# Optimization experiments

Hardware: AMD Instinct MI355X
Metric: run time of the kernel (lower is better)

## Reference

```python
import jax, jax.numpy as jnp
import numpy as np

D_MODEL = 1024


def bitlinear(x, weight):
    # ternary quantization with straight-through estimator; forward value is w_q*scale
    scale = jnp.clip(jnp.mean(jnp.abs(weight), axis=1, keepdims=True), 1e-5, None)
    w_q = jnp.clip(jnp.round(weight / scale), -1.0, 1.0)
    w = weight + jax.lax.stop_gradient(w_q * scale - weight)
    return x @ w.T


def rmsnorm(x, w, eps=1e-6):
    return x * jax.lax.rsqrt(jnp.mean(x * x, axis=-1, keepdims=True) + eps) * w


def setup_inputs() -> dict:
    key = jax.random.key(0)
    ks = jax.random.split(key, 6)
    D = D_MODEL
    std = np.sqrt(2.0 / D)  # kaiming_normal fan_out
    return {
        "x": jax.random.normal(ks[0], (4, 4096, D), dtype=jnp.float32),
        "Wr": jax.random.normal(ks[1], (D, D), dtype=jnp.float32) * std,
        "Wk": jax.random.normal(ks[2], (D, D), dtype=jnp.float32) * std,
        "Wv": jax.random.normal(ks[3], (D, D), dtype=jnp.float32) * std,
        "Wo": jax.random.normal(ks[4], (D, D), dtype=jnp.float32) * std,
        "decay": jnp.ones((D,), dtype=jnp.float32) * 0.99,
        "ln_w": jnp.ones((D,), dtype=jnp.float32),
    }


def reference(x, Wr, Wk, Wv, Wo, decay, ln_w):
    B, T, D = x.shape
    r = jax.nn.sigmoid(bitlinear(x, Wr))
    k = bitlinear(x, Wk)
    v = bitlinear(x, Wv)
    dec = jax.nn.sigmoid(decay)                              # [D]
    kv = k * v                                               # [B,T,D]
    positions = jnp.arange(T, dtype=x.dtype)                 # [T]
    log_decay = jnp.log(jnp.clip(dec, 1e-7, None))           # [D]
    scale = jnp.exp(positions[:, None] * log_decay[None, :])  # [T,D]
    scaled = kv / jnp.clip(scale, 1e-10, None)[None]         # [B,T,D]
    cum = jnp.cumsum(scaled, axis=1)                         # [B,T,D]
    state = cum * scale[None]                                # [B,T,D]
    return bitlinear(rmsnorm(r * state, ln_w), Wo)
```

## Files before the change

### kernel.cpp

```cpp
#include <hip/hip_runtime.h>

typedef unsigned short u16;
typedef __attribute__((ext_vector_type(8))) short bf16x8;
typedef __attribute__((ext_vector_type(4))) float f32x4;
typedef __attribute__((ext_vector_type(4))) int   i32x4;
typedef __attribute__((ext_vector_type(4))) unsigned short u16x4;

#define DM 1024

__device__ __forceinline__ float bf2f(u16 u){
  union { unsigned int i; float f; } v; v.i = ((unsigned int)u)<<16; return v.f;
}
__device__ __forceinline__ u16 f2bf(float f){
  unsigned int x = __float_as_uint(f);
  return (u16)((x + 0x7FFFu + ((x>>16)&1u)) >> 16);
}

__global__ __launch_bounds__(256)
void quantize_w(const float* __restrict__ W0, const float* __restrict__ W1,
                const float* __restrict__ W2, const float* __restrict__ W3,
                u16* __restrict__ wq, signed char* __restrict__ wq8,
                float* __restrict__ wsc)
{
  const int gr   = blockIdx.x*4 + (threadIdx.x>>6);
  const int lane = threadIdx.x & 63;
  const float* W; int row;
  if (gr < 1024)      { W = W0; row = gr; }
  else if (gr < 3072) { row = (gr-1024)>>1; W = (gr&1) ? W2 : W1; }
  else                { W = W3; row = gr-3072; }
  const float* wr = W + (size_t)row*DM;
  float4 v[4]; float s = 0.f;
  #pragma unroll
  for (int c=0;c<4;c++){
    v[c] = *(const float4*)&wr[c*256 + lane*4];
    s += fabsf(v[c].x)+fabsf(v[c].y)+fabsf(v[c].z)+fabsf(v[c].w);
  }
  #pragma unroll
  for (int off=32; off; off>>=1) s += __shfl_down(s, off);
  s = __shfl(s, 0);
  const float scale = fmaxf(s*(1.f/1024.f), 1e-5f);
  if (lane==0) wsc[gr] = scale;
  if (gr < 3072){
    u16* wo = wq + (size_t)gr*DM;
    #pragma unroll
    for (int c=0;c<4;c++){
      u16x4 q;
      q[0] = f2bf(fminf(fmaxf(rintf(v[c].x/scale),-1.f),1.f));
      q[1] = f2bf(fminf(fmaxf(rintf(v[c].y/scale),-1.f),1.f));
      q[2] = f2bf(fminf(fmaxf(rintf(v[c].z/scale),-1.f),1.f));
      q[3] = f2bf(fminf(fmaxf(rintf(v[c].w/scale),-1.f),1.f));
      *(u16x4*)&wo[c*256 + lane*4] = q;
    }
  } else {
    signed char* wo = wq8 + (size_t)(gr-3072)*DM;
    #pragma unroll
    for (int c=0;c<4;c++){
      const int q0 = (int)rintf(fminf(fmaxf(v[c].x/scale,-1.f),1.f));
      const int q1 = (int)rintf(fminf(fmaxf(v[c].y/scale,-1.f),1.f));
      const int q2 = (int)rintf(fminf(fmaxf(v[c].z/scale,-1.f),1.f));
      const int q3 = (int)rintf(fminf(fmaxf(v[c].w/scale,-1.f),1.f));
      const unsigned int p = (q0&0xFF) | ((q1&0xFF)<<8) | ((q2&0xFF)<<16) | ((unsigned)(q3&0xFF)<<24);
      *(unsigned int*)&wo[c*256 + lane*4] = p;
    }
  }
}

__global__ void cvt_x(const float* __restrict__ x, u16* __restrict__ xb){
  const int i = (blockIdx.x*256 + threadIdx.x)*4;
  float4 v = *(const float4*)&x[i];
  u16x4 o; o[0]=f2bf(v.x); o[1]=f2bf(v.y); o[2]=f2bf(v.z); o[3]=f2bf(v.w);
  *(u16x4*)&xb[i] = o;
}

#define RD(base, off) (*(const bf16x8*)((const char*)(base) + (off)))

__global__ __launch_bounds__(256, 4)
void gemm_rkv(const u16* __restrict__ Ag, const u16* __restrict__ Bq,
              const float* __restrict__ bscale,
              u16* __restrict__ o_r, u16* __restrict__ o_kv)
{
  __shared__ u16 sA[128*64];
  __shared__ u16 sB[128*64];
  const int tid = threadIdx.x, wave = tid>>6, lane = tid&63;
  const int lr = lane&15, lg = lane>>4;
  const int wm = wave>>1, wn = wave&1;
  const int bm0 = blockIdx.x*128, bn0 = blockIdx.y*128;
  constexpr int nt = 16;

  const int r8   = lane>>3;
  const int scol = ((lane&7)<<4) ^ (r8<<4);
  const size_t aoff = (size_t)(bm0 + wave*8 + r8)*2048 + scol;
  const size_t boff = (size_t)(bn0 + wave*8 + r8)*2048 + scol;
  const int ldst = wave*1024;

  const int S = (lr&7)<<4;
  const int koff0 = ((lg<<4)     ) ^ S;
  const int koff1 = (64 + (lg<<4)) ^ S;
  const int arow = (wm*64 + lr)*128;
  const int brow = (wn*64 + lr)*128;

  f32x4 acc[4][4];
  #pragma unroll
  for (int i=0;i<4;i++)
    #pragma unroll
    for (int j=0;j<4;j++) acc[i][j] = (f32x4){0.f,0.f,0.f,0.f};

  for (int t=0; t<nt; ++t){
    #pragma unroll
    for (int q=0;q<4;q++){
      __builtin_amdgcn_global_load_lds(
        (const __attribute__((address_space(1))) void*)((const char*)Ag + aoff + q*65536 + (size_t)t*128),
        (__attribute__((address_space(3))) void*)((char*)sA + ldst + q*4096), 16, 0, 0);
      __builtin_amdgcn_global_load_lds(
        (const __attribute__((address_space(1))) void*)((const char*)Bq + boff + q*65536 + (size_t)t*128),
        (__attribute__((address_space(3))) void*)((char*)sB + ldst + q*4096), 16, 0, 0);
    }
    __syncthreads();
    {
      bf16x8 a[4], b[4];
      #pragma unroll
      for (int m=0;m<4;m++) a[m] = RD(sA, arow + m*2048 + koff0);
      #pragma unroll
      for (int n=0;n<4;n++) b[n] = RD(sB, brow + n*2048 + koff0);
      #pragma unroll
      for (int m=0;m<4;m++)
        #pragma unroll
        for (int n=0;n<4;n++)
          acc[m][n] = __builtin_amdgcn_mfma_f32_16x16x32_bf16(a[m], b[n], acc[m][n], 0,0,0);
      #pragma unroll
      for (int m=0;m<4;m++) a[m] = RD(sA, arow + m*2048 + koff1);
      #pragma unroll
      for (int n=0;n<4;n++) b[n] = RD(sB, brow + n*2048 + koff1);
      #pragma unroll
      for (int m=0;m<4;m++)
        #pragma unroll
        for (int n=0;n<4;n++)
          acc[m][n] = __builtin_amdgcn_mfma_f32_16x16x32_bf16(a[m], b[n], acc[m][n], 0,0,0);
    }
    __syncthreads();
  }

  #pragma unroll
  for (int mi=0; mi<4; ++mi){
    #pragma unroll
    for (int ni=0; ni<4; ++ni){
      const int col = bn0 + wn*64 + ni*16 + lr;
      const float sc = bscale[col];
      const int rowb = bm0 + wm*64 + mi*16 + lg*4;
      const f32x4 a = acc[mi][ni];
      if (bn0 < 1024){
        #pragma unroll
        for (int r2=0;r2<4;r2++){
          const float val = a[r2]*sc;
          o_r[(size_t)(rowb+r2)*DM + col] = f2bf(1.f/(1.f+expf(-val)));
        }
      } else {
        const int dv = (col - 1024) >> 1;
        #pragma unroll
        for (int r2=0;r2<4;r2++){
          const float val = a[r2]*sc;
          const float pr  = val * __shfl_xor(val, 1);
          if (!(lr & 1))
            o_kv[(size_t)(rowb+r2)*DM + dv] = f2bf(pr);
        }
      }
    }
  }
}

#define RD8(base, off) (*(const i32x4*)((const char*)(base) + (off)))

__global__ __launch_bounds__(256, 4)
void gemm_o8(const signed char* __restrict__ Ag, const signed char* __restrict__ Bq,
             const float* __restrict__ bscale, const float* __restrict__ sxr,
             float* __restrict__ o_f)
{
  __shared__ signed char sA[128*128];
  __shared__ signed char sB[128*128];
  const int tid = threadIdx.x, wave = tid>>6, lane = tid&63;
  const int lr = lane&15, lg = lane>>4;
  const int wm = wave>>1, wn = wave&1;
  const int bm0 = blockIdx.x*128, bn0 = blockIdx.y*128;
  constexpr int nt = 8;

  const int r8   = lane>>3;
  const int scol = ((lane&7)<<4) ^ (r8<<4);
  const size_t aoff = (size_t)(bm0 + wave*8 + r8)*1024 + scol;
  const size_t boff = (size_t)(bn0 + wave*8 + r8)*1024 + scol;
  const int ldst = wave*1024;

  const int S = (lr&7)<<4;
  const int koff0 = ((lg<<4)     ) ^ S;
  const int koff1 = (64 + (lg<<4)) ^ S;
  const int arow = (wm*64 + lr)*128;
  const int brow = (wn*64 + lr)*128;

  i32x4 acc[4][4];
  #pragma unroll
  for (int i=0;i<4;i++)
    #pragma unroll
    for (int j=0;j<4;j++) acc[i][j] = (i32x4){0,0,0,0};

  for (int t=0; t<nt; ++t){
    #pragma unroll
    for (int q=0;q<4;q++){
      __builtin_amdgcn_global_load_lds(
        (const __attribute__((address_space(1))) void*)((const char*)Ag + aoff + q*32768 + (size_t)t*128),
        (__attribute__((address_space(3))) void*)((char*)sA + ldst + q*4096), 16, 0, 0);
      __builtin_amdgcn_global_load_lds(
        (const __attribute__((address_space(1))) void*)((const char*)Bq + boff + q*32768 + (size_t)t*128),
        (__attribute__((address_space(3))) void*)((char*)sB + ldst + q*4096), 16, 0, 0);
    }
    __syncthreads();
    {
      i32x4 a[4], b[4];
      #pragma unroll
      for (int m=0;m<4;m++) a[m] = RD8(sA, arow + m*2048 + koff0);
      #pragma unroll
      for (int n=0;n<4;n++) b[n] = RD8(sB, brow + n*2048 + koff0);
      #pragma unroll
      for (int m=0;m<4;m++)
        #pragma unroll
        for (int n=0;n<4;n++)
          acc[m][n] = __builtin_amdgcn_mfma_i32_16x16x64_i8(a[m], b[n], acc[m][n], 0,0,0);
      #pragma unroll
      for (int m=0;m<4;m++) a[m] = RD8(sA, arow + m*2048 + koff1);
      #pragma unroll
      for (int n=0;n<4;n++) b[n] = RD8(sB, brow + n*2048 + koff1);
      #pragma unroll
      for (int m=0;m<4;m++)
        #pragma unroll
        for (int n=0;n<4;n++)
          acc[m][n] = __builtin_amdgcn_mfma_i32_16x16x64_i8(a[m], b[n], acc[m][n], 0,0,0);
    }
    __syncthreads();
  }

  #pragma unroll
  for (int mi=0; mi<4; ++mi){
    const int rowb = bm0 + wm*64 + mi*16 + lg*4;
    float sx[4];
    #pragma unroll
    for (int r2=0;r2<4;r2++) sx[r2] = sxr[rowb+r2];
    #pragma unroll
    for (int ni=0; ni<4; ++ni){
      const int col = bn0 + wn*64 + ni*16 + lr;
      const float sc = bscale[col];
      const i32x4 a = acc[mi][ni];
      #pragma unroll
      for (int r2=0;r2<4;r2++)
        o_f[(size_t)(rowb+r2)*DM + col] = (float)a[r2] * sx[r2] * sc;
    }
  }
}

__global__ __launch_bounds__(256)
void kv_phase1(const u16* __restrict__ kv, const float* __restrict__ decay,
               float* __restrict__ part)
{
  const int c = blockIdx.x & 127, b = blockIdx.x >> 7;
  const int d0 = threadIdx.x*4;
  float ld[4]; f32x4 sum = {0.f,0.f,0.f,0.f};
  #pragma unroll
  for (int j=0;j<4;j++){
    const float dec = 1.f/(1.f+expf(-decay[d0+j]));
    ld[j] = logf(fmaxf(dec, 1e-7f));
  }
  for (int t=c*32; t<c*32+32; ++t){
    const size_t base = ((size_t)(b*4096 + t))*DM + d0;
    const u16x4 p4 = *(const u16x4*)&kv[base];
    const float tf = (float)t;
    #pragma unroll
    for (int j=0;j<4;j++){
      const float e = expf(tf*ld[j]);
      sum[j] += bf2f(p4[j]) / fmaxf(e, 1e-10f);
    }
  }
  *(f32x4*)&part[((size_t)(b*128+c))*DM + d0] = sum;
}

__global__ void chunk_prefix(float* __restrict__ part){
  const int g = blockIdx.x*256 + threadIdx.x;
  const int b = g >> 10, d = g & 1023;
  float run = 0.f;
  for (int c8=0; c8<128; c8+=8){
    float v[8];
    #pragma unroll
    for (int i=0;i<8;i++)
      v[i] = part[((size_t)(b*128+c8+i))*DM + d];
    #pragma unroll
    for (int i=0;i<8;i++){
      const float tmp = v[i];
      part[((size_t)(b*128+c8+i))*DM + d] = run;
      run += tmp;
    }
  }
}

__global__ __launch_bounds__(256)
void scan_norm(const u16* __restrict__ kv, const u16* __restrict__ rbuf,
               const float* __restrict__ part, const float* __restrict__ decay,
               const float* __restrict__ lnw, signed char* __restrict__ yn8,
               float* __restrict__ sxr)
{
  const int c = blockIdx.x & 127, b = blockIdx.x >> 7;
  const int tid = threadIdx.x, lane = tid&63, wave = tid>>6;
  const int d0 = tid*4;
  __shared__ float redS[2][4];
  __shared__ float redM[2][4];
  f32x4 run = *(const f32x4*)&part[((size_t)(b*128+c))*DM + d0];
  float ld[4], lw[4];
  #pragma unroll
  for (int j=0;j<4;j++){
    const float dec = 1.f/(1.f+expf(-decay[d0+j]));
    ld[j] = logf(fmaxf(dec, 1e-7f));
    lw[j] = lnw[d0+j];
  }
  for (int t=c*32; t<c*32+32; ++t){
    const size_t base = ((size_t)(b*4096+t))*DM + d0;
    const u16x4 p4 = *(const u16x4*)&kv[base];
    const u16x4 r4 = *(const u16x4*)&rbuf[base];
    const float tf = (float)t;
    float yl[4]; float ss = 0.f, mx = 0.f;
    #pragma unroll
    for (int j=0;j<4;j++){
      const float e = expf(tf*ld[j]);
      run[j] += bf2f(p4[j]) / fmaxf(e, 1e-10f);
      const float st = run[j]*e;
      const float y = bf2f(r4[j])*st;
      ss += y*y;
      yl[j] = y*lw[j];
      mx = fmaxf(mx, fabsf(yl[j]));
    }
    #pragma unroll
    for (int off=32; off; off>>=1){
      ss += __shfl_down(ss, off);
      mx  = fmaxf(mx, __shfl_down(mx, off));
    }
    if (lane==0){ redS[t&1][wave] = ss; redM[t&1][wave] = mx; }
    __builtin_amdgcn_s_barrier();
    const float tot = (redS[t&1][0]+redS[t&1][1])+(redS[t&1][2]+redS[t&1][3]);
    const float m1  = fmaxf(fmaxf(redM[t&1][0],redM[t&1][1]),
                            fmaxf(redM[t&1][2],redM[t&1][3]));
    const float rs  = 1.f/sqrtf(tot*(1.f/1024.f) + 1e-6f);
    const float m1s = fmaxf(m1, 1e-30f);
    const float qk  = 127.f/m1s;
    if (tid==0) sxr[b*4096+t] = m1s*rs*(1.f/127.f);
    unsigned int p = 0;
    #pragma unroll
    for (int j=0;j<4;j++){
      int q = (int)rintf(yl[j]*qk);
      q = q>127?127:(q<-127?-127:q);
      p |= ((unsigned)(q&0xFF)) << (8*j);
    }
    *(unsigned int*)&yn8[base] = p;
  }
}

extern "C" void kernel_launch(void* const* d_in, const int* in_sizes, int n_in,
                              void* d_out, int out_size, void* d_ws, size_t ws_size,
                              hipStream_t stream)
{
  (void)in_sizes; (void)n_in; (void)out_size; (void)ws_size;
  const float* x    = (const float*)d_in[0];
  const float* Wr   = (const float*)d_in[1];
  const float* Wk   = (const float*)d_in[2];
  const float* Wv   = (const float*)d_in[3];
  const float* Wo   = (const float*)d_in[4];
  const float* dec  = (const float*)d_in[5];
  const float* lnw  = (const float*)d_in[6];

  char* ws = (char*)d_ws;
  u16*         wq    = (u16*)(ws + 0);
  signed char* wq8   = (signed char*)(ws + 6291456);
  float*       wsc   = (float*)(ws + 7340032);
  u16*         rbuf  = (u16*)(ws + 7356416);
  u16*         kvbuf = (u16*)(ws + 40910848);
  float*       part  = (float*)(ws + 74465280);
  u16*         xb    = (u16*)(ws + 76562432);
  signed char* yn8   = (signed char*)(ws + 110116864);
  float*       sxr   = (float*)(ws + 126894080);

  quantize_w<<<1024, 256, 0, stream>>>(Wr, Wk, Wv, Wo, wq, wq8, wsc);
  cvt_x<<<16384, 256, 0, stream>>>(x, xb);
  gemm_rkv<<<dim3(128,24), 256, 0, stream>>>(xb, wq, wsc, rbuf, kvbuf);
  kv_phase1<<<512, 256, 0, stream>>>(kvbuf, dec, part);
  chunk_prefix<<<16, 256, 0, stream>>>(part);
  scan_norm<<<512, 256, 0, stream>>>(kvbuf, rbuf, part, dec, lnw, yn8, sxr);
  gemm_o8<<<dim3(128,8), 256, 0, stream>>>(yn8, wq8, wsc + 3072, sxr, (float*)d_out);
}
```

Before: 221.6 us.

## Fuse chunk partial sums into GEMM epilogue and merge weight/x packing launches

Computes the per-32-timestep decayed kv chunk sums directly in the gemm_rkv epilogue using shuffle reductions, which removes the kv_phase1 kernel and its re-read of the kv buffer. It also merges weight quantization and x bf16 conversion into one launch. The epilogue now runs extra expf and divide work per element and adds register pressure in a kernel bounded at 4 waves per SIMD. Summation order changes slightly because it uses bf16-unrounded products rather than the stored bf16 values.

```diff
diff --git a/kernel.cpp b/kernel.cpp
--- a/kernel.cpp
+++ b/kernel.cpp
@@ -17,11 +17,19 @@
 }
 
 __global__ __launch_bounds__(256)
-void quantize_w(const float* __restrict__ W0, const float* __restrict__ W1,
-                const float* __restrict__ W2, const float* __restrict__ W3,
-                u16* __restrict__ wq, signed char* __restrict__ wq8,
-                float* __restrict__ wsc)
-{
+void init_pack(const float* __restrict__ W0, const float* __restrict__ W1,
+               const float* __restrict__ W2, const float* __restrict__ W3,
+               const float* __restrict__ x,
+               u16* __restrict__ wq, signed char* __restrict__ wq8,
+               float* __restrict__ wsc, u16* __restrict__ xb)
+{
+  if (blockIdx.x >= 1024){
+    const int i = ((blockIdx.x-1024)*256 + threadIdx.x)*4;
+    float4 v = *(const float4*)&x[i];
+    u16x4 o; o[0]=f2bf(v.x); o[1]=f2bf(v.y); o[2]=f2bf(v.z); o[3]=f2bf(v.w);
+    *(u16x4*)&xb[i] = o;
+    return;
+  }
   const int gr   = blockIdx.x*4 + (threadIdx.x>>6);
   const int lane = threadIdx.x & 63;
   const float* W; int row;
@@ -65,19 +73,13 @@
   }
 }
 
-__global__ void cvt_x(const float* __restrict__ x, u16* __restrict__ xb){
-  const int i = (blockIdx.x*256 + threadIdx.x)*4;
-  float4 v = *(const float4*)&x[i];
-  u16x4 o; o[0]=f2bf(v.x); o[1]=f2bf(v.y); o[2]=f2bf(v.z); o[3]=f2bf(v.w);
-  *(u16x4*)&xb[i] = o;
-}
-
 #define RD(base, off) (*(const bf16x8*)((const char*)(base) + (off)))
 
 __global__ __launch_bounds__(256, 4)
 void gemm_rkv(const u16* __restrict__ Ag, const u16* __restrict__ Bq,
-              const float* __restrict__ bscale,
-              u16* __restrict__ o_r, u16* __restrict__ o_kv)
+              const float* __restrict__ bscale, const float* __restrict__ decay,
+              u16* __restrict__ o_r, u16* __restrict__ o_kv,
+              float* __restrict__ part)
 {
   __shared__ u16 sA[128*64];
   __shared__ u16 sB[128*64];
@@ -141,28 +143,48 @@
   }
 
   #pragma unroll
-  for (int mi=0; mi<4; ++mi){
-    #pragma unroll
-    for (int ni=0; ni<4; ++ni){
-      const int col = bn0 + wn*64 + ni*16 + lr;
-      const float sc = bscale[col];
-      const int rowb = bm0 + wm*64 + mi*16 + lg*4;
-      const f32x4 a = acc[mi][ni];
-      if (bn0 < 1024){
+  for (int ni=0; ni<4; ++ni){
+    const int col = bn0 + wn*64 + ni*16 + lr;
+    const float sc = bscale[col];
+    if (bn0 < 1024){
+      #pragma unroll
+      for (int mi=0; mi<4; ++mi){
+        const int rowb = bm0 + wm*64 + mi*16 + lg*4;
+        const f32x4 a = acc[mi][ni];
         #pragma unroll
         for (int r2=0;r2<4;r2++){
           const float val = a[r2]*sc;
           o_r[(size_t)(rowb+r2)*DM + col] = f2bf(1.f/(1.f+expf(-val)));
         }
-      } else {
-        const int dv = (col - 1024) >> 1;
+      }
+    } else {
+      const int dv  = (col - 1024) >> 1;
+      const float dec = 1.f/(1.f+expf(-decay[dv]));
+      const float ldv = logf(fmaxf(dec, 1e-7f));
+      float s0 = 0.f, s1 = 0.f;
+      #pragma unroll
+      for (int mi=0; mi<4; ++mi){
+        const int rowb = bm0 + wm*64 + mi*16 + lg*4;
+        const f32x4 a = acc[mi][ni];
         #pragma unroll
         for (int r2=0;r2<4;r2++){
           const float val = a[r2]*sc;
           const float pr  = val * __shfl_xor(val, 1);
           if (!(lr & 1))
             o_kv[(size_t)(rowb+r2)*DM + dv] = f2bf(pr);
+          const int tt = (rowb & 4095) + r2;
+          const float e = expf((float)tt * ldv);
+          const float sv = pr / fmaxf(e, 1e-10f);
+          if (mi < 2) s0 += sv; else s1 += sv;
         }
+      }
+      s0 += __shfl_down(s0, 32); s0 += __shfl_down(s0, 16);
+      s1 += __shfl_down(s1, 32); s1 += __shfl_down(s1, 16);
+      if ((lane < 16) && !(lane & 1)){
+        const int bb = bm0 >> 12;
+        const int c0 = ((bm0 & 4095) + wm*64) >> 5;
+        part[((size_t)(bb*128 + c0    ))*DM + dv] = s0;
+        part[((size_t)(bb*128 + c0 + 1))*DM + dv] = s1;
       }
     }
   }
@@ -252,31 +274,6 @@
         o_f[(size_t)(rowb+r2)*DM + col] = (float)a[r2] * sx[r2] * sc;
     }
   }
-}
-
-__global__ __launch_bounds__(256)
-void kv_phase1(const u16* __restrict__ kv, const float* __restrict__ decay,
-               float* __restrict__ part)
-{
-  const int c = blockIdx.x & 127, b = blockIdx.x >> 7;
-  const int d0 = threadIdx.x*4;
-  float ld[4]; f32x4 sum = {0.f,0.f,0.f,0.f};
-  #pragma unroll
-  for (int j=0;j<4;j++){
-    const float dec = 1.f/(1.f+expf(-decay[d0+j]));
-    ld[j] = logf(fmaxf(dec, 1e-7f));
-  }
-  for (int t=c*32; t<c*32+32; ++t){
-    const size_t base = ((size_t)(b*4096 + t))*DM + d0;
-    const u16x4 p4 = *(const u16x4*)&kv[base];
-    const float tf = (float)t;
-    #pragma unroll
-    for (int j=0;j<4;j++){
-      const float e = expf(tf*ld[j]);
-      sum[j] += bf2f(p4[j]) / fmaxf(e, 1e-10f);
-    }
-  }
-  *(f32x4*)&part[((size_t)(b*128+c))*DM + d0] = sum;
 }
 
 __global__ void chunk_prefix(float* __restrict__ part){
@@ -381,10 +378,8 @@
   signed char* yn8   = (signed char*)(ws + 110116864);
   float*       sxr   = (float*)(ws + 126894080);
 
-  quantize_w<<<1024, 256, 0, stream>>>(Wr, Wk, Wv, Wo, wq, wq8, wsc);
-  cvt_x<<<16384, 256, 0, stream>>>(x, xb);
-  gemm_rkv<<<dim3(128,24), 256, 0, stream>>>(xb, wq, wsc, rbuf, kvbuf);
-  kv_phase1<<<512, 256, 0, stream>>>(kvbuf, dec, part);
+  init_pack<<<17408, 256, 0, stream>>>(Wr, Wk, Wv, Wo, x, wq, wq8, wsc, xb);
+  gemm_rkv<<<dim3(128,24), 256, 0, stream>>>(xb, wq, wsc, dec, rbuf, kvbuf, part);
   chunk_prefix<<<16, 256, 0, stream>>>(part);
   scan_norm<<<512, 256, 0, stream>>>(kvbuf, rbuf, part, dec, lnw, yn8, sxr);
   gemm_o8<<<dim3(128,8), 256, 0, stream>>>(yn8, wq8, wsc + 3072, sxr, (float*)d_out);
```

Result: slower. 227.4 us (+2.6%).
